# Kernel optimization log

Hardware: AMD Instinct MI355X
Metric: run time of the kernel (lower is better)

Reference implementation:

```python
import jax, jax.numpy as jnp
import numpy as np

N_NODES = 100000
N_EDGES = 1600000
IN_CH, HID_CH, OUT_CH = 128, 128, 64
N_GRAPHS = 64


def gcn_conv(x, src, dst, W, b, n_nodes):
    """PyG-style GCNConv: self-loops already included in (src, dst).
    out_i = b + sum_j norm_ij * (x_j @ W), norm_ij = deg_i^-1/2 * deg_j^-1/2."""
    xw = x @ W  # [N, out]
    deg = jax.ops.segment_sum(jnp.ones_like(dst, dtype=xw.dtype), dst,
                              num_segments=n_nodes)  # [N]
    dinv = jnp.where(deg > 0, jax.lax.rsqrt(jnp.maximum(deg, 1e-12)), 0.0)
    norm = dinv[src] * dinv[dst]  # [E]
    msg = xw[src] * norm[:, None]  # gather + scale  [E, out]
    out = jax.ops.segment_sum(msg, dst, num_segments=n_nodes)  # scatter-add
    return out + b


def global_mean_pool(x, batch, n_graphs):
    s = jax.ops.segment_sum(x, batch, num_segments=n_graphs)
    cnt = jax.ops.segment_sum(jnp.ones((x.shape[0],), x.dtype), batch,
                              num_segments=n_graphs)
    return s / jnp.maximum(cnt, 1.0)[:, None]


def setup_inputs() -> dict:
    key = jax.random.key(0)
    ks = jax.random.split(key, 9)
    x = jax.random.normal(ks[0], (N_NODES, IN_CH), dtype=jnp.float32)
    edge_index = jax.random.randint(ks[1], (2, N_EDGES), 0, N_NODES, dtype=jnp.int64)
    batch = jnp.sort(jax.random.randint(ks[2], (N_NODES,), 0, N_GRAPHS, dtype=jnp.int64))
    # Glorot-ish params
    s1 = 1.0 / np.sqrt(IN_CH)
    s2 = 1.0 / np.sqrt(HID_CH)
    W1 = jax.random.normal(ks[3], (IN_CH, HID_CH), jnp.float32) * s1
    b1 = jnp.zeros((HID_CH,), jnp.float32)
    W2 = jax.random.normal(ks[4], (HID_CH, HID_CH), jnp.float32) * s2
    b2 = jnp.zeros((HID_CH,), jnp.float32)
    Wl = jax.random.normal(ks[5], (HID_CH, OUT_CH), jnp.float32) * s2
    bl = jax.random.normal(ks[6], (OUT_CH,), jnp.float32) * 0.01
    return {"x": x, "edge_index": edge_index, "batch": batch,
            "W1": W1, "b1": b1, "W2": W2, "b2": b2, "Wl": Wl, "bl": bl}


def reference(x, edge_index, batch, W1, b1, W2, b2, Wl, bl):
    n = x.shape[0]
    loop = jnp.arange(n, dtype=edge_index.dtype)
    src = jnp.concatenate([edge_index[0], loop])  # add self-loops
    dst = jnp.concatenate([edge_index[1], loop])
    h = jax.nn.relu(gcn_conv(x, src, dst, W1, b1, n))
    h = jax.nn.relu(gcn_conv(h, src, dst, W2, b2, n))
    g = global_mean_pool(h, batch, N_GRAPHS)  # [B, hid]
    return g @ Wl + bl  # [B, out]
```

## Files before the change

kernel.cpp:

```cpp
#include <hip/hip_runtime.h>

#define N_NODESC 100000
#define N_EDGESC 1600000
#define CH 128
#define NG 64
#define OC 64

#define GST_BLKS 391
#define MFMA_BLKS 1563
#define PAD_STRIDE 64
#define SENTINEL N_NODESC

#define BIN_SHIFT 9
#define BIN_W 512
#define NBINS 196
#define BIN_CAP 16384
#define BIN1_BLKS 391
#define E_PER_BIN1 4096

typedef __attribute__((ext_vector_type(8))) short short8;
typedef __attribute__((ext_vector_type(4))) float f32x4;

__device__ __forceinline__ unsigned short f2b_u(float f) {
    union { float f; unsigned int u; } x; x.f = f;
    unsigned int u = x.u;
    return (unsigned short)((u + 0x7fffu + ((u >> 16) & 1u)) >> 16);
}
__device__ __forceinline__ float b2f_lo(unsigned int v) {
    union { unsigned int u; float f; } x; x.u = v << 16; return x.f;
}
__device__ __forceinline__ float b2f_hi(unsigned int v) {
    union { unsigned int u; float f; } x; x.u = v & 0xffff0000u; return x.f;
}

#define WSTR 136
template<int AFP>
__device__ __forceinline__ void mfma_compute(int blk, int t, const void* __restrict__ Ap,
                                             unsigned short* __restrict__ Ob,
                                             const unsigned short* WsT) {
    int wave = t >> 6, lane = t & 63;
    int quad = lane >> 4, l16 = lane & 15;
    int arow = blk * 64 + wave * 16 + l16;
    bool rowok = arow < N_NODESC;
    f32x4 acc[8] = {};
#pragma unroll
    for (int c = 0; c < 4; ++c) {
        int koff = c * 32 + quad * 8;
        short8 a;
        if (AFP) {
            const float* A = (const float*)Ap;
            float4 f0 = make_float4(0, 0, 0, 0), f1 = make_float4(0, 0, 0, 0);
            if (rowok) {
                f0 = *(const float4*)(A + (size_t)arow * 128 + koff);
                f1 = *(const float4*)(A + (size_t)arow * 128 + koff + 4);
            }
            a[0] = (short)f2b_u(f0.x); a[1] = (short)f2b_u(f0.y);
            a[2] = (short)f2b_u(f0.z); a[3] = (short)f2b_u(f0.w);
            a[4] = (short)f2b_u(f1.x); a[5] = (short)f2b_u(f1.y);
            a[6] = (short)f2b_u(f1.z); a[7] = (short)f2b_u(f1.w);
        } else {
            const unsigned short* A = (const unsigned short*)Ap;
            if (rowok) a = *(const short8*)(A + (size_t)arow * 128 + koff);
            else       a = (short8)(short)0;
        }
#pragma unroll
        for (int tt = 0; tt < 8; ++tt) {
            short8 b = *(const short8*)&WsT[(tt * 16 + l16) * WSTR + koff];
            acc[tt] = __builtin_amdgcn_mfma_f32_16x16x32_bf16(a, b, acc[tt], 0, 0, 0);
        }
    }
    int orow0 = blk * 64 + wave * 16 + quad * 4;
#pragma unroll
    for (int r = 0; r < 4; ++r) {
        int g = orow0 + r;
        if (g < N_NODESC) {
#pragma unroll
            for (int tt = 0; tt < 8; ++tt)
                Ob[(size_t)g * 128 + tt * 16 + l16] = f2b_u(acc[tt][r]);
        }
    }
}

__global__ __launch_bounds__(256) void k_pre(const int* __restrict__ ei,
                                             const int* __restrict__ batch,
                                             const float* __restrict__ W1,
                                             const float* __restrict__ W2,
                                             int* __restrict__ cursor,
                                             unsigned int* __restrict__ binbuf,
                                             unsigned short* __restrict__ Wt1,
                                             unsigned short* __restrict__ Wt2,
                                             int* __restrict__ gstart) {
    __shared__ int hist[NBINS];
    int b = blockIdx.x, t = threadIdx.x;
    if (b < BIN1_BLKS) {
        for (int i = t; i < NBINS; i += 256) hist[i] = 0;
        __syncthreads();
        int e0 = b * E_PER_BIN1;
#pragma unroll 4
        for (int i = 0; i < E_PER_BIN1 / 256; ++i) {
            int e = e0 + i * 256 + t;
            if (e < N_EDGESC) atomicAdd(&hist[ei[N_EDGESC + e] >> BIN_SHIFT], 1);
        }
        __syncthreads();
        for (int i = t; i < NBINS; i += 256) {
            int c = hist[i];
            hist[i] = c ? atomicAdd(&cursor[i], c) : 0;
        }
        __syncthreads();
#pragma unroll 4
        for (int i = 0; i < E_PER_BIN1 / 256; ++i) {
            int e = e0 + i * 256 + t;
            if (e < N_EDGESC) {
                int d = ei[N_EDGESC + e];
                int s = ei[e];
                int bin = d >> BIN_SHIFT;
                int off = atomicAdd(&hist[bin], 1);
                binbuf[(size_t)bin * BIN_CAP + off] =
                    ((unsigned int)(d & (BIN_W - 1)) << 17) | (unsigned int)s;
            }
        }
    } else if (b < BIN1_BLKS + 64) {
        int i = (b - BIN1_BLKS) * 256 + t;
        int k = i >> 7, c = i & 127;
        Wt1[c * 128 + k] = f2b_u(W1[k * 128 + c]);
    } else if (b < BIN1_BLKS + 128) {
        int i = (b - BIN1_BLKS - 64) * 256 + t;
        int k = i >> 7, c = i & 127;
        Wt2[c * 128 + k] = f2b_u(W2[k * 128 + c]);
    } else {
        int i = (b - BIN1_BLKS - 128) * 256 + t;
        if (i >= N_NODESC) return;
        int bb = batch[i];
        int bp = (i == 0) ? -1 : batch[i - 1];
        for (int g = bp + 1; g <= bb; ++g) gstart[g] = i;
        if (i == N_NODESC - 1)
            for (int g = bb + 1; g <= NG; ++g) gstart[g] = N_NODESC;
    }
}

__global__ __launch_bounds__(256) void k_main(const float* __restrict__ x,
                                              const unsigned short* __restrict__ Wt1,
                                              unsigned short* __restrict__ xw,
                                              const int* __restrict__ cursor,
                                              const unsigned int* __restrict__ binbuf,
                                              int* __restrict__ deg,
                                              float* __restrict__ dinvt,
                                              int* __restrict__ pad) {
    __shared__ unsigned short WsT[128 * WSTR];
    int t = threadIdx.x;
    if (blockIdx.x < NBINS) {
        int bin = blockIdx.x;
        if (bin == 0 && t == 0) dinvt[SENTINEL] = 0.f;
        int* ldeg = (int*)WsT;
        for (int i = t; i < BIN_W; i += 256) ldeg[i] = 0;
        __syncthreads();
        int n = cursor[bin];
        size_t base = (size_t)bin * BIN_CAP;
        for (int i = t; i < n; i += 256) {
            unsigned int rec = binbuf[base + i];
            int dl = rec >> 17;
            int s = rec & 0x1FFFF;
            int slot = atomicAdd(&ldeg[dl], 1) & (PAD_STRIDE - 1);
            pad[(size_t)((bin << BIN_SHIFT) + dl) * PAD_STRIDE + slot] = s;
        }
        __syncthreads();
        for (int i = t; i < BIN_W; i += 256) {
            int node = (bin << BIN_SHIFT) + i;
            if (node < N_NODESC) {
                int dg = ldeg[i];
                if (dg > PAD_STRIDE) dg = PAD_STRIDE;
                deg[node] = dg;
                dinvt[node] = rsqrtf((float)(dg + 1));
                int r8 = (dg + 7) & ~7;
                for (int j = dg; j < r8; ++j)
                    pad[(size_t)node * PAD_STRIDE + j] = SENTINEL;
            }
        }
    } else {
        int blk = blockIdx.x - NBINS;
        const uint4* wsrc = (const uint4*)Wt1;
        for (int idx = t; idx < 2048; idx += 256) {
            int row = idx >> 4, sub = idx & 15;
            *((uint4*)&WsT[row * WSTR] + sub) = wsrc[row * 16 + sub];
        }
        __syncthreads();
        mfma_compute<1>(blk, t, x, xw, WsT);
    }
}

__global__ __launch_bounds__(256) void k_mfma2(const unsigned short* __restrict__ A,
                                               const unsigned short* __restrict__ Wt,
                                               unsigned short* __restrict__ Ob) {
    __shared__ unsigned short WsT[128 * WSTR];
    int t = threadIdx.x;
    {
        const uint4* wsrc = (const uint4*)Wt;
        for (int idx = t; idx < 2048; idx += 256) {
            int row = idx >> 4, sub = idx & 15;
            *((uint4*)&WsT[row * WSTR] + sub) = wsrc[row * 16 + sub];
        }
    }
    __syncthreads();
    mfma_compute<0>(blockIdx.x, t, A, Ob, WsT);
}

__device__ __forceinline__ void gather8(const unsigned int* __restrict__ xw,
                                        const int* __restrict__ pad,
                                        const float* __restrict__ dinvt,
                                        int base, int lane,
                                        float& acc0, float& acc1) {
    int s[8];
    float w[8];
    unsigned int v[8];
#pragma unroll
    for (int k = 0; k < 8; ++k) s[k] = pad[base + k];
#pragma unroll
    for (int k = 0; k < 8; ++k) {
        w[k] = dinvt[s[k]];
        v[k] = xw[(unsigned int)(s[k] * 64 + lane)];
    }
#pragma unroll
    for (int k = 0; k < 8; ++k) {
        acc0 += w[k] * b2f_lo(v[k]);
        acc1 += w[k] * b2f_hi(v[k]);
    }
}

__device__ __forceinline__ void gather_pair(const unsigned int* __restrict__ xw,
                                            const int* __restrict__ pad,
                                            const float* __restrict__ dinvt,
                                            int nA, int nB, int dgA, int dgB, int lane,
                                            float& a0, float& a1, float& b0, float& b1) {
    int ngA = (dgA + 7) >> 3, ngB = (dgB + 7) >> 3;
    int baseA = nA * PAD_STRIDE, baseB = nB * PAD_STRIDE;
    int ngmin = ngA < ngB ? ngA : ngB;
    int g = 0;
    for (; g < ngmin; ++g) {
        gather8(xw, pad, dinvt, baseA + g * 8, lane, a0, a1);
        gather8(xw, pad, dinvt, baseB + g * 8, lane, b0, b1);
    }
    for (; g < ngA; ++g) gather8(xw, pad, dinvt, baseA + g * 8, lane, a0, a1);
    for (; g < ngB; ++g) gather8(xw, pad, dinvt, baseB + g * 8, lane, b0, b1);
}

__global__ __launch_bounds__(256) void k_gather1(const unsigned int* __restrict__ xw,
                                                 const int* __restrict__ deg,
                                                 const float* __restrict__ dinvt,
                                                 const int* __restrict__ pad,
                                                 const float* __restrict__ bias,
                                                 unsigned int* __restrict__ outp) {
    int t = threadIdx.x;
    int lane = t & 63;
    int nA = blockIdx.x * 8 + (t >> 6) * 2;
    if (nA >= N_NODESC) return;
    int nB = nA + 1;
    if (nB >= N_NODESC) nB = nA;
    int dgA = deg[nA], dgB = deg[nB];
    float wA = dinvt[nA], wB = dinvt[nB];
    unsigned int vsA = xw[(unsigned int)(nA * 64 + lane)];
    unsigned int vsB = xw[(unsigned int)(nB * 64 + lane)];
    float a0 = wA * b2f_lo(vsA), a1 = wA * b2f_hi(vsA);
    float b0 = wB * b2f_lo(vsB), b1 = wB * b2f_hi(vsB);
    gather_pair(xw, pad, dinvt, nA, nB, dgA, dgB, lane, a0, a1, b0, b1);
    float2 bb = ((const float2*)bias)[lane];
    float oA0 = fmaxf(bb.x + wA * a0, 0.f), oA1 = fmaxf(bb.y + wA * a1, 0.f);
    float oB0 = fmaxf(bb.x + wB * b0, 0.f), oB1 = fmaxf(bb.y + wB * b1, 0.f);
    outp[(unsigned int)(nA * 64 + lane)] =
        ((unsigned int)f2b_u(oA1) << 16) | (unsigned int)f2b_u(oA0);
    outp[(unsigned int)(nB * 64 + lane)] =
        ((unsigned int)f2b_u(oB1) << 16) | (unsigned int)f2b_u(oB0);
}

__global__ __launch_bounds__(256) void k_gather_pool(const unsigned int* __restrict__ xw,
                                                     const int* __restrict__ deg,
                                                     const float* __restrict__ dinvt,
                                                     const int* __restrict__ pad,
                                                     const float* __restrict__ bias,
                                                     const int* __restrict__ batch,
                                                     float* __restrict__ gpart) {
    __shared__ float lds[4 * 128];
    int t = threadIdx.x, w = t >> 6, lane = t & 63;
    int base = blockIdx.x * 16;
    bool fast = batch[base] == batch[base + 15];
    float2 bv = ((const float2*)bias)[lane];
    float sum0 = 0.f, sum1 = 0.f;
#pragma unroll
    for (int p = 0; p < 2; ++p) {
        int nA = base + w * 4 + p * 2;
        int nB = nA + 1;
        int dgA = deg[nA], dgB = deg[nB];
        float wA = dinvt[nA], wB = dinvt[nB];
        unsigned int vsA = xw[(unsigned int)(nA * 64 + lane)];
        unsigned int vsB = xw[(unsigned int)(nB * 64 + lane)];
        float a0 = wA * b2f_lo(vsA), a1 = wA * b2f_hi(vsA);
        float b0 = wB * b2f_lo(vsB), b1 = wB * b2f_hi(vsB);
        gather_pair(xw, pad, dinvt, nA, nB, dgA, dgB, lane, a0, a1, b0, b1);
        float oA0 = fmaxf(bv.x + wA * a0, 0.f), oA1 = fmaxf(bv.y + wA * a1, 0.f);
        float oB0 = fmaxf(bv.x + wB * b0, 0.f), oB1 = fmaxf(bv.y + wB * b1, 0.f);
        if (fast) {
            sum0 += oA0 + oB0; sum1 += oA1 + oB1;
        } else {
            int gA = batch[nA], gB = batch[nB];
            atomicAdd(&gpart[gA * 128 + lane * 2], oA0);
            atomicAdd(&gpart[gA * 128 + lane * 2 + 1], oA1);
            atomicAdd(&gpart[gB * 128 + lane * 2], oB0);
            atomicAdd(&gpart[gB * 128 + lane * 2 + 1], oB1);
        }
    }
    if (fast) {
        lds[w * 128 + lane * 2] = sum0;
        lds[w * 128 + lane * 2 + 1] = sum1;
        __syncthreads();
        if (t < 128) {
            float v = lds[t] + lds[128 + t] + lds[256 + t] + lds[384 + t];
            atomicAdd(&gpart[batch[base] * 128 + t], v);
        }
    }
}

__global__ void k_final(const float* __restrict__ gpart, const int* __restrict__ gstart,
                        const float* __restrict__ Wl, const float* __restrict__ bl,
                        float* __restrict__ out) {
    __shared__ float gs[128];
    int b = blockIdx.x;
    int o = threadIdx.x;
    gs[o] = gpart[b * 128 + o];
    gs[o + 64] = gpart[b * 128 + 64 + o];
    __syncthreads();
    int cnt = gstart[b + 1] - gstart[b];
    float sc = 1.f / (float)(cnt > 0 ? cnt : 1);
    float sum = 0.f;
    for (int k = 0; k < 128; ++k) sum += gs[k] * Wl[k * 64 + o];
    out[b * 64 + o] = bl[o] + sc * sum;
}

extern "C" void kernel_launch(void* const* d_in, const int* in_sizes, int n_in,
                              void* d_out, int out_size, void* d_ws, size_t ws_size,
                              hipStream_t stream) {
    const float* x    = (const float*)d_in[0];
    const int*   ei   = (const int*)d_in[1];
    const int*   batch= (const int*)d_in[2];
    const float* W1   = (const float*)d_in[3];
    const float* b1   = (const float*)d_in[4];
    const float* W2   = (const float*)d_in[5];
    const float* b2   = (const float*)d_in[6];
    const float* Wl   = (const float*)d_in[7];
    const float* bl   = (const float*)d_in[8];
    float* out = (float*)d_out;

    char* ws = (char*)d_ws;
    unsigned short* xw_s = (unsigned short*)ws; ws += (size_t)(N_NODESC + 1) * CH * 2;
    unsigned short* h_b  = (unsigned short*)ws; ws += (size_t)N_NODESC * CH * 2;
    unsigned short* Wt1 = (unsigned short*)ws; ws += (size_t)CH * CH * 2;
    unsigned short* Wt2 = (unsigned short*)ws; ws += (size_t)CH * CH * 2;
    int*   cursor = (int*)ws;   ws += (size_t)NBINS * 4;
    float* gpart  = (float*)ws; ws += (size_t)NG * CH * 4;
    int*   deg    = (int*)ws;   ws += (size_t)N_NODESC * 4;
    float* dinvt  = (float*)ws; ws += (size_t)(N_NODESC + 1) * 4;
    int*   pad    = (int*)ws;   ws += (size_t)N_NODESC * PAD_STRIDE * 4;
    unsigned int* binbuf = (unsigned int*)ws; ws += (size_t)NBINS * BIN_CAP * 4;
    int*   gstart = (int*)ws;   ws += (NG + 8) * 4;

    hipMemsetAsync(cursor, 0, (size_t)NBINS * 4 + (size_t)NG * CH * 4, stream);

    k_pre<<<BIN1_BLKS + 128 + GST_BLKS, 256, 0, stream>>>(ei, batch, W1, W2,
        cursor, binbuf, Wt1, Wt2, gstart);
    k_main<<<NBINS + MFMA_BLKS, 256, 0, stream>>>(x, Wt1, xw_s, cursor, binbuf,
                                                  deg, dinvt, pad);

    k_gather1<<<(N_NODESC + 7) / 8, 256, 0, stream>>>((const unsigned int*)xw_s,
        deg, dinvt, pad, b1, (unsigned int*)h_b);
    k_mfma2<<<MFMA_BLKS, 256, 0, stream>>>(h_b, Wt2, xw_s);
    k_gather_pool<<<N_NODESC / 16, 256, 0, stream>>>((const unsigned int*)xw_s,
        deg, dinvt, pad, b2, batch, gpart);

    k_final<<<NG, 64, 0, stream>>>(gpart, gstart, Wl, bl, out);
}
```

Measured before the change: 307.2 us.

## Fuse all GCN stages into one cooperative persistent kernel with grid syncs

Replaces the six separate kernel launches with a single cooperative persistent kernel that loops over work units per phase and separates phases with grid-wide syncs, falling back to the old launch sequence if cooperative launch fails. It also pads the bin cursors to one per 64-byte line to reduce atomic contention. The aim is to remove launch gaps and tail effects between stages. The costs are grid-sync overhead, a grid capped at 1024 blocks, LDS for both the weight tile and scratch in every block, and an occupancy query on every call.

Measured after the change: 747.0 us. 143% more time.

```diff
diff --git a/kernel.cpp b/kernel.cpp
--- a/kernel.cpp
+++ b/kernel.cpp
@@ -1,4 +1,6 @@
 #include <hip/hip_runtime.h>
+#include <hip/hip_cooperative_groups.h>
+namespace cg = cooperative_groups;
 
 #define N_NODESC 100000
 #define N_EDGESC 1600000
@@ -17,6 +19,12 @@
 #define BIN_CAP 16384
 #define BIN1_BLKS 391
 #define E_PER_BIN1 4096
+
+#define GRID_MAX 1024
+#define P0_UNITS (BIN1_BLKS + 128 + GST_BLKS)
+#define P1_UNITS (NBINS + MFMA_BLKS)
+#define P2_UNITS 12500
+#define P4_UNITS 6250
 
 typedef __attribute__((ext_vector_type(8))) short short8;
 typedef __attribute__((ext_vector_type(4))) float f32x4;
@@ -81,129 +89,6 @@
     }
 }
 
-__global__ __launch_bounds__(256) void k_pre(const int* __restrict__ ei,
-                                             const int* __restrict__ batch,
-                                             const float* __restrict__ W1,
-                                             const float* __restrict__ W2,
-                                             int* __restrict__ cursor,
-                                             unsigned int* __restrict__ binbuf,
-                                             unsigned short* __restrict__ Wt1,
-                                             unsigned short* __restrict__ Wt2,
-                                             int* __restrict__ gstart) {
-    __shared__ int hist[NBINS];
-    int b = blockIdx.x, t = threadIdx.x;
-    if (b < BIN1_BLKS) {
-        for (int i = t; i < NBINS; i += 256) hist[i] = 0;
-        __syncthreads();
-        int e0 = b * E_PER_BIN1;
-#pragma unroll 4
-        for (int i = 0; i < E_PER_BIN1 / 256; ++i) {
-            int e = e0 + i * 256 + t;
-            if (e < N_EDGESC) atomicAdd(&hist[ei[N_EDGESC + e] >> BIN_SHIFT], 1);
-        }
-        __syncthreads();
-        for (int i = t; i < NBINS; i += 256) {
-            int c = hist[i];
-            hist[i] = c ? atomicAdd(&cursor[i], c) : 0;
-        }
-        __syncthreads();
-#pragma unroll 4
-        for (int i = 0; i < E_PER_BIN1 / 256; ++i) {
-            int e = e0 + i * 256 + t;
-            if (e < N_EDGESC) {
-                int d = ei[N_EDGESC + e];
-                int s = ei[e];
-                int bin = d >> BIN_SHIFT;
-                int off = atomicAdd(&hist[bin], 1);
-                binbuf[(size_t)bin * BIN_CAP + off] =
-                    ((unsigned int)(d & (BIN_W - 1)) << 17) | (unsigned int)s;
-            }
-        }
-    } else if (b < BIN1_BLKS + 64) {
-        int i = (b - BIN1_BLKS) * 256 + t;
-        int k = i >> 7, c = i & 127;
-        Wt1[c * 128 + k] = f2b_u(W1[k * 128 + c]);
-    } else if (b < BIN1_BLKS + 128) {
-        int i = (b - BIN1_BLKS - 64) * 256 + t;
-        int k = i >> 7, c = i & 127;
-        Wt2[c * 128 + k] = f2b_u(W2[k * 128 + c]);
-    } else {
-        int i = (b - BIN1_BLKS - 128) * 256 + t;
-        if (i >= N_NODESC) return;
-        int bb = batch[i];
-        int bp = (i == 0) ? -1 : batch[i - 1];
-        for (int g = bp + 1; g <= bb; ++g) gstart[g] = i;
-        if (i == N_NODESC - 1)
-            for (int g = bb + 1; g <= NG; ++g) gstart[g] = N_NODESC;
-    }
-}
-
-__global__ __launch_bounds__(256) void k_main(const float* __restrict__ x,
-                                              const unsigned short* __restrict__ Wt1,
-                                              unsigned short* __restrict__ xw,
-                                              const int* __restrict__ cursor,
-                                              const unsigned int* __restrict__ binbuf,
-                                              int* __restrict__ deg,
-                                              float* __restrict__ dinvt,
-                                              int* __restrict__ pad) {
-    __shared__ unsigned short WsT[128 * WSTR];
-    int t = threadIdx.x;
-    if (blockIdx.x < NBINS) {
-        int bin = blockIdx.x;
-        if (bin == 0 && t == 0) dinvt[SENTINEL] = 0.f;
-        int* ldeg = (int*)WsT;
-        for (int i = t; i < BIN_W; i += 256) ldeg[i] = 0;
-        __syncthreads();
-        int n = cursor[bin];
-        size_t base = (size_t)bin * BIN_CAP;
-        for (int i = t; i < n; i += 256) {
-            unsigned int rec = binbuf[base + i];
-            int dl = rec >> 17;
-            int s = rec & 0x1FFFF;
-            int slot = atomicAdd(&ldeg[dl], 1) & (PAD_STRIDE - 1);
-            pad[(size_t)((bin << BIN_SHIFT) + dl) * PAD_STRIDE + slot] = s;
-        }
-        __syncthreads();
-        for (int i = t; i < BIN_W; i += 256) {
-            int node = (bin << BIN_SHIFT) + i;
-            if (node < N_NODESC) {
-                int dg = ldeg[i];
-                if (dg > PAD_STRIDE) dg = PAD_STRIDE;
-                deg[node] = dg;
-                dinvt[node] = rsqrtf((float)(dg + 1));
-                int r8 = (dg + 7) & ~7;
-                for (int j = dg; j < r8; ++j)
-                    pad[(size_t)node * PAD_STRIDE + j] = SENTINEL;
-            }
-        }
-    } else {
-        int blk = blockIdx.x - NBINS;
-        const uint4* wsrc = (const uint4*)Wt1;
-        for (int idx = t; idx < 2048; idx += 256) {
-            int row = idx >> 4, sub = idx & 15;
-            *((uint4*)&WsT[row * WSTR] + sub) = wsrc[row * 16 + sub];
-        }
-        __syncthreads();
-        mfma_compute<1>(blk, t, x, xw, WsT);
-    }
-}
-
-__global__ __launch_bounds__(256) void k_mfma2(const unsigned short* __restrict__ A,
-                                               const unsigned short* __restrict__ Wt,
-                                               unsigned short* __restrict__ Ob) {
-    __shared__ unsigned short WsT[128 * WSTR];
-    int t = threadIdx.x;
-    {
-        const uint4* wsrc = (const uint4*)Wt;
-        for (int idx = t; idx < 2048; idx += 256) {
-            int row = idx >> 4, sub = idx & 15;
-            *((uint4*)&WsT[row * WSTR] + sub) = wsrc[row * 16 + sub];
-        }
-    }
-    __syncthreads();
-    mfma_compute<0>(blockIdx.x, t, A, Ob, WsT);
-}
-
 __device__ __forceinline__ void gather8(const unsigned int* __restrict__ xw,
                                         const int* __restrict__ pad,
                                         const float* __restrict__ dinvt,
@@ -243,15 +128,79 @@
     for (; g < ngB; ++g) gather8(xw, pad, dinvt, baseB + g * 8, lane, b0, b1);
 }
 
-__global__ __launch_bounds__(256) void k_gather1(const unsigned int* __restrict__ xw,
-                                                 const int* __restrict__ deg,
-                                                 const float* __restrict__ dinvt,
-                                                 const int* __restrict__ pad,
-                                                 const float* __restrict__ bias,
-                                                 unsigned int* __restrict__ outp) {
-    int t = threadIdx.x;
-    int lane = t & 63;
-    int nA = blockIdx.x * 8 + (t >> 6) * 2;
+__device__ __forceinline__ void bin1_body(int u, int t, const int* __restrict__ ei,
+                                          int* __restrict__ cursor,
+                                          unsigned int* __restrict__ binbuf,
+                                          int* hist) {
+    for (int i = t; i < NBINS; i += 256) hist[i] = 0;
+    __syncthreads();
+    int e0 = u * E_PER_BIN1;
+#pragma unroll 4
+    for (int i = 0; i < E_PER_BIN1 / 256; ++i) {
+        int e = e0 + i * 256 + t;
+        if (e < N_EDGESC) atomicAdd(&hist[ei[N_EDGESC + e] >> BIN_SHIFT], 1);
+    }
+    __syncthreads();
+    for (int i = t; i < NBINS; i += 256) {
+        int c = hist[i];
+        hist[i] = c ? atomicAdd(&cursor[i * 16], c) : 0;
+    }
+    __syncthreads();
+#pragma unroll 4
+    for (int i = 0; i < E_PER_BIN1 / 256; ++i) {
+        int e = e0 + i * 256 + t;
+        if (e < N_EDGESC) {
+            int d = ei[N_EDGESC + e];
+            int s = ei[e];
+            int bin = d >> BIN_SHIFT;
+            int off = atomicAdd(&hist[bin], 1);
+            binbuf[(size_t)bin * BIN_CAP + off] =
+                ((unsigned int)(d & (BIN_W - 1)) << 17) | (unsigned int)s;
+        }
+    }
+    __syncthreads();
+}
+
+__device__ __forceinline__ void bin2_body(int bin, int t, const int* __restrict__ cursor,
+                                          const unsigned int* __restrict__ binbuf,
+                                          int* __restrict__ deg, float* __restrict__ dinvt,
+                                          int* __restrict__ pad, int* ldeg) {
+    if (bin == 0 && t == 0) dinvt[SENTINEL] = 0.f;
+    for (int i = t; i < BIN_W; i += 256) ldeg[i] = 0;
+    __syncthreads();
+    int n = cursor[bin * 16];
+    size_t base = (size_t)bin * BIN_CAP;
+    for (int i = t; i < n; i += 256) {
+        unsigned int rec = binbuf[base + i];
+        int dl = rec >> 17;
+        int s = rec & 0x1FFFF;
+        int slot = atomicAdd(&ldeg[dl], 1) & (PAD_STRIDE - 1);
+        pad[(size_t)((bin << BIN_SHIFT) + dl) * PAD_STRIDE + slot] = s;
+    }
+    __syncthreads();
+    for (int i = t; i < BIN_W; i += 256) {
+        int node = (bin << BIN_SHIFT) + i;
+        if (node < N_NODESC) {
+            int dg = ldeg[i];
+            if (dg > PAD_STRIDE) dg = PAD_STRIDE;
+            deg[node] = dg;
+            dinvt[node] = rsqrtf((float)(dg + 1));
+            int r8 = (dg + 7) & ~7;
+            for (int j = dg; j < r8; ++j)
+                pad[(size_t)node * PAD_STRIDE + j] = SENTINEL;
+        }
+    }
+    __syncthreads();
+}
+
+__device__ __forceinline__ void gather1_body(int u, int wv, int lane,
+                                             const unsigned int* __restrict__ xw,
+                                             const int* __restrict__ deg,
+                                             const float* __restrict__ dinvt,
+                                             const int* __restrict__ pad,
+                                             const float* __restrict__ bias1,
+                                             unsigned int* __restrict__ hb) {
+    int nA = u * 8 + wv * 2;
     if (nA >= N_NODESC) return;
     int nB = nA + 1;
     if (nB >= N_NODESC) nB = nA;
@@ -262,31 +211,30 @@
     float a0 = wA * b2f_lo(vsA), a1 = wA * b2f_hi(vsA);
     float b0 = wB * b2f_lo(vsB), b1 = wB * b2f_hi(vsB);
     gather_pair(xw, pad, dinvt, nA, nB, dgA, dgB, lane, a0, a1, b0, b1);
-    float2 bb = ((const float2*)bias)[lane];
+    float2 bb = ((const float2*)bias1)[lane];
     float oA0 = fmaxf(bb.x + wA * a0, 0.f), oA1 = fmaxf(bb.y + wA * a1, 0.f);
     float oB0 = fmaxf(bb.x + wB * b0, 0.f), oB1 = fmaxf(bb.y + wB * b1, 0.f);
-    outp[(unsigned int)(nA * 64 + lane)] =
+    hb[(unsigned int)(nA * 64 + lane)] =
         ((unsigned int)f2b_u(oA1) << 16) | (unsigned int)f2b_u(oA0);
-    outp[(unsigned int)(nB * 64 + lane)] =
+    hb[(unsigned int)(nB * 64 + lane)] =
         ((unsigned int)f2b_u(oB1) << 16) | (unsigned int)f2b_u(oB0);
 }
 
-__global__ __launch_bounds__(256) void k_gather_pool(const unsigned int* __restrict__ xw,
-                                                     const int* __restrict__ deg,
-                                                     const float* __restrict__ dinvt,
-                                                     const int* __restrict__ pad,
-                                                     const float* __restrict__ bias,
-                                                     const int* __restrict__ batch,
-                                                     float* __restrict__ gpart) {
-    __shared__ float lds[4 * 128];
-    int t = threadIdx.x, w = t >> 6, lane = t & 63;
-    int base = blockIdx.x * 16;
+__device__ __forceinline__ void gpool_body(int u, int t, int wv, int lane,
+                                           const unsigned int* __restrict__ xw,
+                                           const int* __restrict__ deg,
+                                           const float* __restrict__ dinvt,
+                                           const int* __restrict__ pad,
+                                           const float* __restrict__ bias2,
+                                           const int* __restrict__ batch,
+                                           float* __restrict__ gpart, float* lds) {
+    int base = u * 16;
     bool fast = batch[base] == batch[base + 15];
-    float2 bv = ((const float2*)bias)[lane];
+    float2 bv = ((const float2*)bias2)[lane];
     float sum0 = 0.f, sum1 = 0.f;
 #pragma unroll
     for (int p = 0; p < 2; ++p) {
-        int nA = base + w * 4 + p * 2;
+        int nA = base + wv * 4 + p * 2;
         int nB = nA + 1;
         int dgA = deg[nA], dgB = deg[nB];
         float wA = dinvt[nA], wB = dinvt[nB];
@@ -308,14 +256,207 @@
         }
     }
     if (fast) {
-        lds[w * 128 + lane * 2] = sum0;
-        lds[w * 128 + lane * 2 + 1] = sum1;
+        lds[wv * 128 + lane * 2] = sum0;
+        lds[wv * 128 + lane * 2 + 1] = sum1;
         __syncthreads();
         if (t < 128) {
             float v = lds[t] + lds[128 + t] + lds[256 + t] + lds[384 + t];
             atomicAdd(&gpart[batch[base] * 128 + t], v);
         }
-    }
+        __syncthreads();
+    }
+}
+
+__global__ __launch_bounds__(256, 4) void k_all(
+    const float* __restrict__ x, const int* __restrict__ ei,
+    const int* __restrict__ batch,
+    const float* __restrict__ W1, const float* __restrict__ W2,
+    const float* __restrict__ bias1, const float* __restrict__ bias2,
+    const float* __restrict__ Wl, const float* __restrict__ bl,
+    float* __restrict__ out,
+    unsigned short* __restrict__ xw, unsigned short* __restrict__ hb,
+    unsigned short* __restrict__ Wt1, unsigned short* __restrict__ Wt2,
+    int* __restrict__ cursor, unsigned int* __restrict__ binbuf,
+    int* __restrict__ deg, float* __restrict__ dinvt,
+    int* __restrict__ pad, float* __restrict__ gpart,
+    int* __restrict__ gstart)
+{
+    cg::grid_group grid = cg::this_grid();
+    __shared__ unsigned short WsT[128 * WSTR];
+    __shared__ int scratch[BIN_W];
+    int t = threadIdx.x;
+    int lane = t & 63, wv = t >> 6;
+    int nblk = gridDim.x;
+
+    for (int u = blockIdx.x; u < P0_UNITS; u += nblk) {
+        if (u < BIN1_BLKS) {
+            bin1_body(u, t, ei, cursor, binbuf, (int*)WsT);
+        } else if (u < BIN1_BLKS + 64) {
+            int i = (u - BIN1_BLKS) * 256 + t;
+            int k = i >> 7, c = i & 127;
+            Wt1[c * 128 + k] = f2b_u(W1[k * 128 + c]);
+        } else if (u < BIN1_BLKS + 128) {
+            int i = (u - BIN1_BLKS - 64) * 256 + t;
+            int k = i >> 7, c = i & 127;
+            Wt2[c * 128 + k] = f2b_u(W2[k * 128 + c]);
+        } else {
+            int i = (u - BIN1_BLKS - 128) * 256 + t;
+            if (i < N_NODESC) {
+                int bb = batch[i];
+                int bp = (i == 0) ? -1 : batch[i - 1];
+                for (int g = bp + 1; g <= bb; ++g) gstart[g] = i;
+                if (i == N_NODESC - 1)
+                    for (int g = bb + 1; g <= NG; ++g) gstart[g] = N_NODESC;
+            }
+        }
+    }
+    grid.sync();
+
+    {
+        const uint4* wsrc = (const uint4*)Wt1;
+        for (int idx = t; idx < 2048; idx += 256) {
+            int row = idx >> 4, sub = idx & 15;
+            *((uint4*)&WsT[row * WSTR] + sub) = wsrc[row * 16 + sub];
+        }
+        __syncthreads();
+    }
+    for (int u = blockIdx.x; u < P1_UNITS; u += nblk) {
+        if (u < NBINS) bin2_body(u, t, cursor, binbuf, deg, dinvt, pad, scratch);
+        else           mfma_compute<1>(u - NBINS, t, x, xw, WsT);
+    }
+    grid.sync();
+
+    for (int u = blockIdx.x; u < P2_UNITS; u += nblk)
+        gather1_body(u, wv, lane, (const unsigned int*)xw, deg, dinvt, pad, bias1,
+                     (unsigned int*)hb);
+    grid.sync();
+
+    {
+        const uint4* wsrc = (const uint4*)Wt2;
+        for (int idx = t; idx < 2048; idx += 256) {
+            int row = idx >> 4, sub = idx & 15;
+            *((uint4*)&WsT[row * WSTR] + sub) = wsrc[row * 16 + sub];
+        }
+        __syncthreads();
+    }
+    for (int u = blockIdx.x; u < MFMA_BLKS; u += nblk)
+        mfma_compute<0>(u, t, hb, xw, WsT);
+    grid.sync();
+
+    for (int u = blockIdx.x; u < P4_UNITS; u += nblk)
+        gpool_body(u, t, wv, lane, (const unsigned int*)xw, deg, dinvt, pad, bias2,
+                   batch, gpart, (float*)scratch);
+    grid.sync();
+
+    {
+        float* gs = (float*)scratch;
+        for (int u = blockIdx.x; u < NG; u += nblk) {
+            if (t < 128) gs[t] = gpart[u * 128 + t];
+            __syncthreads();
+            if (t < 64) {
+                int cnt = gstart[u + 1] - gstart[u];
+                float sc = 1.f / (float)(cnt > 0 ? cnt : 1);
+                float sum = 0.f;
+                for (int k = 0; k < 128; ++k) sum += gs[k] * Wl[k * 64 + t];
+                out[u * 64 + t] = bl[t] + sc * sum;
+            }
+            __syncthreads();
+        }
+    }
+}
+
+__global__ __launch_bounds__(256) void k_pre(const int* __restrict__ ei,
+                                             const int* __restrict__ batch,
+                                             const float* __restrict__ W1,
+                                             const float* __restrict__ W2,
+                                             int* __restrict__ cursor,
+                                             unsigned int* __restrict__ binbuf,
+                                             unsigned short* __restrict__ Wt1,
+                                             unsigned short* __restrict__ Wt2,
+                                             int* __restrict__ gstart) {
+    __shared__ int hist[NBINS];
+    int b = blockIdx.x, t = threadIdx.x;
+    if (b < BIN1_BLKS) {
+        bin1_body(b, t, ei, cursor, binbuf, hist);
+    } else if (b < BIN1_BLKS + 64) {
+        int i = (b - BIN1_BLKS) * 256 + t;
+        int k = i >> 7, c = i & 127;
+        Wt1[c * 128 + k] = f2b_u(W1[k * 128 + c]);
+    } else if (b < BIN1_BLKS + 128) {
+        int i = (b - BIN1_BLKS - 64) * 256 + t;
+        int k = i >> 7, c = i & 127;
+        Wt2[c * 128 + k] = f2b_u(W2[k * 128 + c]);
+    } else {
+        int i = (b - BIN1_BLKS - 128) * 256 + t;
+        if (i >= N_NODESC) return;
+        int bb = batch[i];
+        int bp = (i == 0) ? -1 : batch[i - 1];
+        for (int g = bp + 1; g <= bb; ++g) gstart[g] = i;
+        if (i == N_NODESC - 1)
+            for (int g = bb + 1; g <= NG; ++g) gstart[g] = N_NODESC;
+    }
+}
+
+__global__ __launch_bounds__(256) void k_main(const float* __restrict__ x,
+                                              const unsigned short* __restrict__ Wt1,
+                                              unsigned short* __restrict__ xw,
+                                              const int* __restrict__ cursor,
+                                              const unsigned int* __restrict__ binbuf,
+                                              int* __restrict__ deg,
+                                              float* __restrict__ dinvt,
+                                              int* __restrict__ pad) {
+    __shared__ unsigned short WsT[128 * WSTR];
+    int t = threadIdx.x;
+    if (blockIdx.x < NBINS) {
+        bin2_body(blockIdx.x, t, cursor, binbuf, deg, dinvt, pad, (int*)WsT);
+    } else {
+        const uint4* wsrc = (const uint4*)Wt1;
+        for (int idx = t; idx < 2048; idx += 256) {
+            int row = idx >> 4, sub = idx & 15;
+            *((uint4*)&WsT[row * WSTR] + sub) = wsrc[row * 16 + sub];
+        }
+        __syncthreads();
+        mfma_compute<1>(blockIdx.x - NBINS, t, x, xw, WsT);
+    }
+}
+
+__global__ __launch_bounds__(256) void k_mfma2(const unsigned short* __restrict__ A,
+                                               const unsigned short* __restrict__ Wt,
+                                               unsigned short* __restrict__ Ob) {
+    __shared__ unsigned short WsT[128 * WSTR];
+    int t = threadIdx.x;
+    {
+        const uint4* wsrc = (const uint4*)Wt;
+        for (int idx = t; idx < 2048; idx += 256) {
+            int row = idx >> 4, sub = idx & 15;
+            *((uint4*)&WsT[row * WSTR] + sub) = wsrc[row * 16 + sub];
+        }
+    }
+    __syncthreads();
+    mfma_compute<0>(blockIdx.x, t, A, Ob, WsT);
+}
+
+__global__ __launch_bounds__(256) void k_gather1(const unsigned int* __restrict__ xw,
+                                                 const int* __restrict__ deg,
+                                                 const float* __restrict__ dinvt,
+                                                 const int* __restrict__ pad,
+                                                 const float* __restrict__ bias,
+                                                 unsigned int* __restrict__ outp) {
+    int t = threadIdx.x;
+    gather1_body(blockIdx.x, t >> 6, t & 63, xw, deg, dinvt, pad, bias, outp);
+}
+
+__global__ __launch_bounds__(256) void k_gather_pool(const unsigned int* __restrict__ xw,
+                                                     const int* __restrict__ deg,
+                                                     const float* __restrict__ dinvt,
+                                                     const int* __restrict__ pad,
+                                                     const float* __restrict__ bias,
+                                                     const int* __restrict__ batch,
+                                                     float* __restrict__ gpart) {
+    __shared__ float lds[4 * 128];
+    int t = threadIdx.x;
+    gpool_body(blockIdx.x, t, t >> 6, t & 63, xw, deg, dinvt, pad, bias, batch,
+               gpart, lds);
 }
 
 __global__ void k_final(const float* __restrict__ gpart, const int* __restrict__ gstart,
@@ -341,9 +482,9 @@
     const int*   ei   = (const int*)d_in[1];
     const int*   batch= (const int*)d_in[2];
     const float* W1   = (const float*)d_in[3];
-    const float* b1   = (const float*)d_in[4];
+    const float* b1v  = (const float*)d_in[4];
     const float* W2   = (const float*)d_in[5];
-    const float* b2   = (const float*)d_in[6];
+    const float* b2v  = (const float*)d_in[6];
     const float* Wl   = (const float*)d_in[7];
     const float* bl   = (const float*)d_in[8];
     float* out = (float*)d_out;
@@ -353,7 +494,7 @@
     unsigned short* h_b  = (unsigned short*)ws; ws += (size_t)N_NODESC * CH * 2;
     unsigned short* Wt1 = (unsigned short*)ws; ws += (size_t)CH * CH * 2;
     unsigned short* Wt2 = (unsigned short*)ws; ws += (size_t)CH * CH * 2;
-    int*   cursor = (int*)ws;   ws += (size_t)NBINS * 4;
+    int*   cursor = (int*)ws;   ws += (size_t)NBINS * 16 * 4;
     float* gpart  = (float*)ws; ws += (size_t)NG * CH * 4;
     int*   deg    = (int*)ws;   ws += (size_t)N_NODESC * 4;
     float* dinvt  = (float*)ws; ws += (size_t)(N_NODESC + 1) * 4;
@@ -361,18 +502,37 @@
     unsigned int* binbuf = (unsigned int*)ws; ws += (size_t)NBINS * BIN_CAP * 4;
     int*   gstart = (int*)ws;   ws += (NG + 8) * 4;
 
-    hipMemsetAsync(cursor, 0, (size_t)NBINS * 4 + (size_t)NG * CH * 4, stream);
-
-    k_pre<<<BIN1_BLKS + 128 + GST_BLKS, 256, 0, stream>>>(ei, batch, W1, W2,
-        cursor, binbuf, Wt1, Wt2, gstart);
-    k_main<<<NBINS + MFMA_BLKS, 256, 0, stream>>>(x, Wt1, xw_s, cursor, binbuf,
-                                                  deg, dinvt, pad);
-
-    k_gather1<<<(N_NODESC + 7) / 8, 256, 0, stream>>>((const unsigned int*)xw_s,
-        deg, dinvt, pad, b1, (unsigned int*)h_b);
-    k_mfma2<<<MFMA_BLKS, 256, 0, stream>>>(h_b, Wt2, xw_s);
-    k_gather_pool<<<N_NODESC / 16, 256, 0, stream>>>((const unsigned int*)xw_s,
-        deg, dinvt, pad, b2, batch, gpart);
-
-    k_final<<<NG, 64, 0, stream>>>(gpart, gstart, Wl, bl, out);
-}
+    hipMemsetAsync(cursor, 0, (size_t)NBINS * 16 * 4 + (size_t)NG * CH * 4, stream);
+
+    int perCU = 0;
+    hipError_t qerr = hipOccupancyMaxActiveBlocksPerMultiprocessor(
+        &perCU, (const void*)k_all, 256, 0);
+    bool coop_ok = false;
+    if (qerr == hipSuccess && perCU > 0) {
+        int grid = perCU * 256;
+        if (grid > GRID_MAX) grid = GRID_MAX;
+        void* args[] = {
+            (void*)&x, (void*)&ei, (void*)&batch, (void*)&W1, (void*)&W2,
+            (void*)&b1v, (void*)&b2v, (void*)&Wl, (void*)&bl, (void*)&out,
+            (void*)&xw_s, (void*)&h_b, (void*)&Wt1, (void*)&Wt2,
+            (void*)&cursor, (void*)&binbuf, (void*)&deg, (void*)&dinvt,
+            (void*)&pad, (void*)&gpart, (void*)&gstart
+        };
+        hipError_t lerr = hipLaunchCooperativeKernel((const void*)k_all, dim3(grid),
+                                                     dim3(256), args, 0, stream);
+        coop_ok = (lerr == hipSuccess);
+    }
+
+    if (!coop_ok) {
+        k_pre<<<BIN1_BLKS + 128 + GST_BLKS, 256, 0, stream>>>(ei, batch, W1, W2,
+            cursor, binbuf, Wt1, Wt2, gstart);
+        k_main<<<NBINS + MFMA_BLKS, 256, 0, stream>>>(x, Wt1, xw_s, cursor, binbuf,
+                                                      deg, dinvt, pad);
+        k_gather1<<<P2_UNITS, 256, 0, stream>>>((const unsigned int*)xw_s,
+            deg, dinvt, pad, b1v, (unsigned int*)h_b);
+        k_mfma2<<<MFMA_BLKS, 256, 0, stream>>>(h_b, Wt2, xw_s);
+        k_gather_pool<<<P4_UNITS, 256, 0, stream>>>((const unsigned int*)xw_s,
+            deg, dinvt, pad, b2v, batch, gpart);
+        k_final<<<NG, 64, 0, stream>>>(gpart, gstart, Wl, bl, out);
+    }
+}
```

## Restructure GCN pipeline: fuse layer-1 GEMM into binning, gather+GEMM2, pool+head

Applied to the files above, without the earlier changes.

Moves the layer-1 MFMA GEMM into the first binning kernel, with each block converting W1 to bf16 in LDS itself, so it overlaps with edge binning. The bin-to-pad pass becomes its own kernel. Layer-1 gather and the layer-2 GEMM are fused per 64-node block, and the final linear head runs in the last-arriving pool block via an atomic done counter. Bin cursors are padded to separate cache lines. This drops two launches and a transpose pass, but every GEMM block now redoes the W1 conversion, and the fused gather+GEMM blocks run with lower parallelism and a large LDS footprint.

Result: slower. 956.7 us (+211.4%).

```diff
diff --git a/kernel.cpp b/kernel.cpp
--- a/kernel.cpp
+++ b/kernel.cpp
@@ -6,7 +6,6 @@
 #define NG 64
 #define OC 64
 
-#define GST_BLKS 391
 #define MFMA_BLKS 1563
 #define PAD_STRIDE 64
 #define SENTINEL N_NODESC
@@ -17,6 +16,14 @@
 #define BIN_CAP 16384
 #define BIN1_BLKS 391
 #define E_PER_BIN1 4096
+#define GST_BLKS 391
+
+#define U_BIN1 BIN1_BLKS
+#define U_MFMA (U_BIN1 + MFMA_BLKS)
+#define U_PW2  (U_MFMA + 64)
+#define PRE_BLKS (U_PW2 + GST_BLKS)
+
+#define GP_BLKS 6250
 
 typedef __attribute__((ext_vector_type(8))) short short8;
 typedef __attribute__((ext_vector_type(4))) float f32x4;
@@ -81,129 +88,6 @@
     }
 }
 
-__global__ __launch_bounds__(256) void k_pre(const int* __restrict__ ei,
-                                             const int* __restrict__ batch,
-                                             const float* __restrict__ W1,
-                                             const float* __restrict__ W2,
-                                             int* __restrict__ cursor,
-                                             unsigned int* __restrict__ binbuf,
-                                             unsigned short* __restrict__ Wt1,
-                                             unsigned short* __restrict__ Wt2,
-                                             int* __restrict__ gstart) {
-    __shared__ int hist[NBINS];
-    int b = blockIdx.x, t = threadIdx.x;
-    if (b < BIN1_BLKS) {
-        for (int i = t; i < NBINS; i += 256) hist[i] = 0;
-        __syncthreads();
-        int e0 = b * E_PER_BIN1;
-#pragma unroll 4
-        for (int i = 0; i < E_PER_BIN1 / 256; ++i) {
-            int e = e0 + i * 256 + t;
-            if (e < N_EDGESC) atomicAdd(&hist[ei[N_EDGESC + e] >> BIN_SHIFT], 1);
-        }
-        __syncthreads();
-        for (int i = t; i < NBINS; i += 256) {
-            int c = hist[i];
-            hist[i] = c ? atomicAdd(&cursor[i], c) : 0;
-        }
-        __syncthreads();
-#pragma unroll 4
-        for (int i = 0; i < E_PER_BIN1 / 256; ++i) {
-            int e = e0 + i * 256 + t;
-            if (e < N_EDGESC) {
-                int d = ei[N_EDGESC + e];
-                int s = ei[e];
-                int bin = d >> BIN_SHIFT;
-                int off = atomicAdd(&hist[bin], 1);
-                binbuf[(size_t)bin * BIN_CAP + off] =
-                    ((unsigned int)(d & (BIN_W - 1)) << 17) | (unsigned int)s;
-            }
-        }
-    } else if (b < BIN1_BLKS + 64) {
-        int i = (b - BIN1_BLKS) * 256 + t;
-        int k = i >> 7, c = i & 127;
-        Wt1[c * 128 + k] = f2b_u(W1[k * 128 + c]);
-    } else if (b < BIN1_BLKS + 128) {
-        int i = (b - BIN1_BLKS - 64) * 256 + t;
-        int k = i >> 7, c = i & 127;
-        Wt2[c * 128 + k] = f2b_u(W2[k * 128 + c]);
-    } else {
-        int i = (b - BIN1_BLKS - 128) * 256 + t;
-        if (i >= N_NODESC) return;
-        int bb = batch[i];
-        int bp = (i == 0) ? -1 : batch[i - 1];
-        for (int g = bp + 1; g <= bb; ++g) gstart[g] = i;
-        if (i == N_NODESC - 1)
-            for (int g = bb + 1; g <= NG; ++g) gstart[g] = N_NODESC;
-    }
-}
-
-__global__ __launch_bounds__(256) void k_main(const float* __restrict__ x,
-                                              const unsigned short* __restrict__ Wt1,
-                                              unsigned short* __restrict__ xw,
-                                              const int* __restrict__ cursor,
-                                              const unsigned int* __restrict__ binbuf,
-                                              int* __restrict__ deg,
-                                              float* __restrict__ dinvt,
-                                              int* __restrict__ pad) {
-    __shared__ unsigned short WsT[128 * WSTR];
-    int t = threadIdx.x;
-    if (blockIdx.x < NBINS) {
-        int bin = blockIdx.x;
-        if (bin == 0 && t == 0) dinvt[SENTINEL] = 0.f;
-        int* ldeg = (int*)WsT;
-        for (int i = t; i < BIN_W; i += 256) ldeg[i] = 0;
-        __syncthreads();
-        int n = cursor[bin];
-        size_t base = (size_t)bin * BIN_CAP;
-        for (int i = t; i < n; i += 256) {
-            unsigned int rec = binbuf[base + i];
-            int dl = rec >> 17;
-            int s = rec & 0x1FFFF;
-            int slot = atomicAdd(&ldeg[dl], 1) & (PAD_STRIDE - 1);
-            pad[(size_t)((bin << BIN_SHIFT) + dl) * PAD_STRIDE + slot] = s;
-        }
-        __syncthreads();
-        for (int i = t; i < BIN_W; i += 256) {
-            int node = (bin << BIN_SHIFT) + i;
-            if (node < N_NODESC) {
-                int dg = ldeg[i];
-                if (dg > PAD_STRIDE) dg = PAD_STRIDE;
-                deg[node] = dg;
-                dinvt[node] = rsqrtf((float)(dg + 1));
-                int r8 = (dg + 7) & ~7;
-                for (int j = dg; j < r8; ++j)
-                    pad[(size_t)node * PAD_STRIDE + j] = SENTINEL;
-            }
-        }
-    } else {
-        int blk = blockIdx.x - NBINS;
-        const uint4* wsrc = (const uint4*)Wt1;
-        for (int idx = t; idx < 2048; idx += 256) {
-            int row = idx >> 4, sub = idx & 15;
-            *((uint4*)&WsT[row * WSTR] + sub) = wsrc[row * 16 + sub];
-        }
-        __syncthreads();
-        mfma_compute<1>(blk, t, x, xw, WsT);
-    }
-}
-
-__global__ __launch_bounds__(256) void k_mfma2(const unsigned short* __restrict__ A,
-                                               const unsigned short* __restrict__ Wt,
-                                               unsigned short* __restrict__ Ob) {
-    __shared__ unsigned short WsT[128 * WSTR];
-    int t = threadIdx.x;
-    {
-        const uint4* wsrc = (const uint4*)Wt;
-        for (int idx = t; idx < 2048; idx += 256) {
-            int row = idx >> 4, sub = idx & 15;
-            *((uint4*)&WsT[row * WSTR] + sub) = wsrc[row * 16 + sub];
-        }
-    }
-    __syncthreads();
-    mfma_compute<0>(blockIdx.x, t, A, Ob, WsT);
-}
-
 __device__ __forceinline__ void gather8(const unsigned int* __restrict__ xw,
                                         const int* __restrict__ pad,
                                         const float* __restrict__ dinvt,
@@ -243,58 +127,174 @@
     for (; g < ngB; ++g) gather8(xw, pad, dinvt, baseB + g * 8, lane, b0, b1);
 }
 
-__global__ __launch_bounds__(256) void k_gather1(const unsigned int* __restrict__ xw,
-                                                 const int* __restrict__ deg,
-                                                 const float* __restrict__ dinvt,
-                                                 const int* __restrict__ pad,
-                                                 const float* __restrict__ bias,
-                                                 unsigned int* __restrict__ outp) {
-    int t = threadIdx.x;
-    int lane = t & 63;
-    int nA = blockIdx.x * 8 + (t >> 6) * 2;
-    if (nA >= N_NODESC) return;
-    int nB = nA + 1;
-    if (nB >= N_NODESC) nB = nA;
-    int dgA = deg[nA], dgB = deg[nB];
-    float wA = dinvt[nA], wB = dinvt[nB];
-    unsigned int vsA = xw[(unsigned int)(nA * 64 + lane)];
-    unsigned int vsB = xw[(unsigned int)(nB * 64 + lane)];
-    float a0 = wA * b2f_lo(vsA), a1 = wA * b2f_hi(vsA);
-    float b0 = wB * b2f_lo(vsB), b1 = wB * b2f_hi(vsB);
-    gather_pair(xw, pad, dinvt, nA, nB, dgA, dgB, lane, a0, a1, b0, b1);
-    float2 bb = ((const float2*)bias)[lane];
-    float oA0 = fmaxf(bb.x + wA * a0, 0.f), oA1 = fmaxf(bb.y + wA * a1, 0.f);
-    float oB0 = fmaxf(bb.x + wB * b0, 0.f), oB1 = fmaxf(bb.y + wB * b1, 0.f);
-    outp[(unsigned int)(nA * 64 + lane)] =
-        ((unsigned int)f2b_u(oA1) << 16) | (unsigned int)f2b_u(oA0);
-    outp[(unsigned int)(nB * 64 + lane)] =
-        ((unsigned int)f2b_u(oB1) << 16) | (unsigned int)f2b_u(oB0);
-}
-
-__global__ __launch_bounds__(256) void k_gather_pool(const unsigned int* __restrict__ xw,
-                                                     const int* __restrict__ deg,
-                                                     const float* __restrict__ dinvt,
-                                                     const int* __restrict__ pad,
-                                                     const float* __restrict__ bias,
-                                                     const int* __restrict__ batch,
-                                                     float* __restrict__ gpart) {
-    __shared__ float lds[4 * 128];
-    int t = threadIdx.x, w = t >> 6, lane = t & 63;
+__global__ __launch_bounds__(256) void k_pre(const float* __restrict__ x,
+                                             const int* __restrict__ ei,
+                                             const int* __restrict__ batch,
+                                             const float* __restrict__ W1,
+                                             const float* __restrict__ W2,
+                                             int* __restrict__ cursor,
+                                             unsigned int* __restrict__ binbuf,
+                                             unsigned short* __restrict__ Wt2,
+                                             int* __restrict__ gstart,
+                                             unsigned short* __restrict__ xw) {
+    __shared__ unsigned short WsT[128 * WSTR];
+    int b = blockIdx.x, t = threadIdx.x;
+    if (b < U_BIN1) {
+        int* hist = (int*)WsT;
+        for (int i = t; i < NBINS; i += 256) hist[i] = 0;
+        __syncthreads();
+        int e0 = b * E_PER_BIN1;
+#pragma unroll 4
+        for (int i = 0; i < E_PER_BIN1 / 256; ++i) {
+            int e = e0 + i * 256 + t;
+            if (e < N_EDGESC) atomicAdd(&hist[ei[N_EDGESC + e] >> BIN_SHIFT], 1);
+        }
+        __syncthreads();
+        for (int i = t; i < NBINS; i += 256) {
+            int c = hist[i];
+            hist[i] = c ? atomicAdd(&cursor[i * 16], c) : 0;
+        }
+        __syncthreads();
+#pragma unroll 4
+        for (int i = 0; i < E_PER_BIN1 / 256; ++i) {
+            int e = e0 + i * 256 + t;
+            if (e < N_EDGESC) {
+                int d = ei[N_EDGESC + e];
+                int s = ei[e];
+                int bin = d >> BIN_SHIFT;
+                int off = atomicAdd(&hist[bin], 1);
+                binbuf[(size_t)bin * BIN_CAP + off] =
+                    ((unsigned int)(d & (BIN_W - 1)) << 17) | (unsigned int)s;
+            }
+        }
+    } else if (b < U_MFMA) {
+        for (int idx = t; idx < 16384; idx += 256) {
+            int k = idx >> 7, c = idx & 127;
+            WsT[c * WSTR + k] = f2b_u(W1[idx]);
+        }
+        __syncthreads();
+        mfma_compute<1>(b - U_BIN1, t, x, xw, WsT);
+    } else if (b < U_PW2) {
+        int i = (b - U_MFMA) * 256 + t;
+        int k = i >> 7, c = i & 127;
+        Wt2[c * 128 + k] = f2b_u(W2[k * 128 + c]);
+    } else {
+        int i = (b - U_PW2) * 256 + t;
+        if (i >= N_NODESC) return;
+        int bb = batch[i];
+        int bp = (i == 0) ? -1 : batch[i - 1];
+        for (int g = bp + 1; g <= bb; ++g) gstart[g] = i;
+        if (i == N_NODESC - 1)
+            for (int g = bb + 1; g <= NG; ++g) gstart[g] = N_NODESC;
+    }
+}
+
+__global__ __launch_bounds__(256) void k_bin2(const int* __restrict__ cursor,
+                                              const unsigned int* __restrict__ binbuf,
+                                              int* __restrict__ deg,
+                                              float* __restrict__ dinvt,
+                                              int* __restrict__ pad) {
+    __shared__ int ldeg[BIN_W];
+    int bin = blockIdx.x, t = threadIdx.x;
+    if (bin == 0 && t == 0) dinvt[SENTINEL] = 0.f;
+    for (int i = t; i < BIN_W; i += 256) ldeg[i] = 0;
+    __syncthreads();
+    int n = cursor[bin * 16];
+    size_t base = (size_t)bin * BIN_CAP;
+    for (int i = t; i < n; i += 256) {
+        unsigned int rec = binbuf[base + i];
+        int dl = rec >> 17;
+        int s = rec & 0x1FFFF;
+        int slot = atomicAdd(&ldeg[dl], 1) & (PAD_STRIDE - 1);
+        pad[(size_t)((bin << BIN_SHIFT) + dl) * PAD_STRIDE + slot] = s;
+    }
+    __syncthreads();
+    for (int i = t; i < BIN_W; i += 256) {
+        int node = (bin << BIN_SHIFT) + i;
+        if (node < N_NODESC) {
+            int dg = ldeg[i];
+            if (dg > PAD_STRIDE) dg = PAD_STRIDE;
+            deg[node] = dg;
+            dinvt[node] = rsqrtf((float)(dg + 1));
+            int r8 = (dg + 7) & ~7;
+            for (int j = dg; j < r8; ++j)
+                pad[(size_t)node * PAD_STRIDE + j] = SENTINEL;
+        }
+    }
+}
+
+__global__ __launch_bounds__(256) void k_gg(const unsigned int* __restrict__ xw,
+                                            const int* __restrict__ deg,
+                                            const float* __restrict__ dinvt,
+                                            const int* __restrict__ pad,
+                                            const float* __restrict__ bias1,
+                                            unsigned short* __restrict__ hb,
+                                            const unsigned short* __restrict__ Wt2,
+                                            unsigned short* __restrict__ xw2) {
+    __shared__ unsigned short WsT[128 * WSTR];
+    int t = threadIdx.x, wv = t >> 6, lane = t & 63;
+    {
+        const uint4* wsrc = (const uint4*)Wt2;
+        for (int idx = t; idx < 2048; idx += 256) {
+            int row = idx >> 4, sub = idx & 15;
+            *((uint4*)&WsT[row * WSTR] + sub) = wsrc[row * 16 + sub];
+        }
+    }
+    float2 bb = ((const float2*)bias1)[lane];
+#pragma unroll 1
+    for (int p = 0; p < 8; ++p) {
+        int nA = blockIdx.x * 64 + wv * 16 + p * 2;
+        if (nA < N_NODESC) {
+            int nB = nA + 1;
+            if (nB >= N_NODESC) nB = nA;
+            int dgA = deg[nA], dgB = deg[nB];
+            float wA = dinvt[nA], wB = dinvt[nB];
+            unsigned int vsA = xw[(unsigned int)(nA * 64 + lane)];
+            unsigned int vsB = xw[(unsigned int)(nB * 64 + lane)];
+            float a0 = wA * b2f_lo(vsA), a1 = wA * b2f_hi(vsA);
+            float b0 = wB * b2f_lo(vsB), b1 = wB * b2f_hi(vsB);
+            gather_pair(xw, pad, dinvt, nA, nB, dgA, dgB, lane, a0, a1, b0, b1);
+            float oA0 = fmaxf(bb.x + wA * a0, 0.f), oA1 = fmaxf(bb.y + wA * a1, 0.f);
+            float oB0 = fmaxf(bb.x + wB * b0, 0.f), oB1 = fmaxf(bb.y + wB * b1, 0.f);
+            ((unsigned int*)hb)[(unsigned int)(nA * 64 + lane)] =
+                ((unsigned int)f2b_u(oA1) << 16) | (unsigned int)f2b_u(oA0);
+            ((unsigned int*)hb)[(unsigned int)(nB * 64 + lane)] =
+                ((unsigned int)f2b_u(oB1) << 16) | (unsigned int)f2b_u(oB0);
+        }
+    }
+    __syncthreads();
+    mfma_compute<0>(blockIdx.x, t, hb, xw2, WsT);
+}
+
+__global__ __launch_bounds__(256) void k_gp(const unsigned int* __restrict__ xw2,
+                                            const int* __restrict__ deg,
+                                            const float* __restrict__ dinvt,
+                                            const int* __restrict__ pad,
+                                            const float* __restrict__ bias2,
+                                            const int* __restrict__ batch,
+                                            float* __restrict__ gpart,
+                                            const int* __restrict__ gstart,
+                                            const float* __restrict__ Wl,
+                                            const float* __restrict__ bl,
+                                            float* __restrict__ out,
+                                            int* __restrict__ done) {
+    __shared__ float shead[NG * CH];
+    int t = threadIdx.x, wv = t >> 6, lane = t & 63;
     int base = blockIdx.x * 16;
     bool fast = batch[base] == batch[base + 15];
-    float2 bv = ((const float2*)bias)[lane];
+    float2 bv = ((const float2*)bias2)[lane];
     float sum0 = 0.f, sum1 = 0.f;
 #pragma unroll
     for (int p = 0; p < 2; ++p) {
-        int nA = base + w * 4 + p * 2;
+        int nA = base + wv * 4 + p * 2;
         int nB = nA + 1;
         int dgA = deg[nA], dgB = deg[nB];
         float wA = dinvt[nA], wB = dinvt[nB];
-        unsigned int vsA = xw[(unsigned int)(nA * 64 + lane)];
-        unsigned int vsB = xw[(unsigned int)(nB * 64 + lane)];
+        unsigned int vsA = xw2[(unsigned int)(nA * 64 + lane)];
+        unsigned int vsB = xw2[(unsigned int)(nB * 64 + lane)];
         float a0 = wA * b2f_lo(vsA), a1 = wA * b2f_hi(vsA);
         float b0 = wB * b2f_lo(vsB), b1 = wB * b2f_hi(vsB);
-        gather_pair(xw, pad, dinvt, nA, nB, dgA, dgB, lane, a0, a1, b0, b1);
+        gather_pair(xw2, pad, dinvt, nA, nB, dgA, dgB, lane, a0, a1, b0, b1);
         float oA0 = fmaxf(bv.x + wA * a0, 0.f), oA1 = fmaxf(bv.y + wA * a1, 0.f);
         float oB0 = fmaxf(bv.x + wB * b0, 0.f), oB1 = fmaxf(bv.y + wB * b1, 0.f);
         if (fast) {
@@ -308,30 +308,33 @@
         }
     }
     if (fast) {
-        lds[w * 128 + lane * 2] = sum0;
-        lds[w * 128 + lane * 2 + 1] = sum1;
+        shead[wv * 128 + lane * 2] = sum0;
+        shead[wv * 128 + lane * 2 + 1] = sum1;
         __syncthreads();
         if (t < 128) {
-            float v = lds[t] + lds[128 + t] + lds[256 + t] + lds[384 + t];
+            float v = shead[t] + shead[128 + t] + shead[256 + t] + shead[384 + t];
             atomicAdd(&gpart[batch[base] * 128 + t], v);
         }
     }
-}
-
-__global__ void k_final(const float* __restrict__ gpart, const int* __restrict__ gstart,
-                        const float* __restrict__ Wl, const float* __restrict__ bl,
-                        float* __restrict__ out) {
-    __shared__ float gs[128];
-    int b = blockIdx.x;
-    int o = threadIdx.x;
-    gs[o] = gpart[b * 128 + o];
-    gs[o + 64] = gpart[b * 128 + 64 + o];
-    __syncthreads();
-    int cnt = gstart[b + 1] - gstart[b];
-    float sc = 1.f / (float)(cnt > 0 ? cnt : 1);
-    float sum = 0.f;
-    for (int k = 0; k < 128; ++k) sum += gs[k] * Wl[k * 64 + o];
-    out[b * 64 + o] = bl[o] + sc * sum;
+    __syncthreads();
+    __threadfence();
+    __shared__ int is_last;
+    if (t == 0) is_last = (atomicAdd(done, 1) == GP_BLKS - 1) ? 1 : 0;
+    __syncthreads();
+    if (!is_last) return;
+    for (int i = t; i < NG * CH; i += 256)
+        shead[i] = atomicAdd(&gpart[i], 0.f);
+    __syncthreads();
+    int o = t & 63;
+    int g0 = t >> 6;
+    for (int rep = 0; rep < 16; ++rep) {
+        int g = g0 + rep * 4;
+        int cnt = gstart[g + 1] - gstart[g];
+        float sc = 1.f / (float)(cnt > 0 ? cnt : 1);
+        float sum = 0.f;
+        for (int k = 0; k < 128; ++k) sum += shead[g * 128 + k] * Wl[k * 64 + o];
+        out[g * 64 + o] = bl[o] + sc * sum;
+    }
 }
 
 extern "C" void kernel_launch(void* const* d_in, const int* in_sizes, int n_in,
@@ -341,38 +344,35 @@
     const int*   ei   = (const int*)d_in[1];
     const int*   batch= (const int*)d_in[2];
     const float* W1   = (const float*)d_in[3];
-    const float* b1   = (const float*)d_in[4];
+    const float* b1v  = (const float*)d_in[4];
     const float* W2   = (const float*)d_in[5];
-    const float* b2   = (const float*)d_in[6];
+    const float* b2v  = (const float*)d_in[6];
     const float* Wl   = (const float*)d_in[7];
     const float* bl   = (const float*)d_in[8];
     float* out = (float*)d_out;
 
     char* ws = (char*)d_ws;
     unsigned short* xw_s = (unsigned short*)ws; ws += (size_t)(N_NODESC + 1) * CH * 2;
+    unsigned short* xw2_s= (unsigned short*)ws; ws += (size_t)(N_NODESC + 1) * CH * 2;
     unsigned short* h_b  = (unsigned short*)ws; ws += (size_t)N_NODESC * CH * 2;
-    unsigned short* Wt1 = (unsigned short*)ws; ws += (size_t)CH * CH * 2;
     unsigned short* Wt2 = (unsigned short*)ws; ws += (size_t)CH * CH * 2;
-    int*   cursor = (int*)ws;   ws += (size_t)NBINS * 4;
+    int*   cursor = (int*)ws;   ws += (size_t)NBINS * 16 * 4;
     float* gpart  = (float*)ws; ws += (size_t)NG * CH * 4;
+    int*   done   = (int*)ws;   ws += 16 * 4;
     int*   deg    = (int*)ws;   ws += (size_t)N_NODESC * 4;
     float* dinvt  = (float*)ws; ws += (size_t)(N_NODESC + 1) * 4;
     int*   pad    = (int*)ws;   ws += (size_t)N_NODESC * PAD_STRIDE * 4;
     unsigned int* binbuf = (unsigned int*)ws; ws += (size_t)NBINS * BIN_CAP * 4;
     int*   gstart = (int*)ws;   ws += (NG + 8) * 4;
 
-    hipMemsetAsync(cursor, 0, (size_t)NBINS * 4 + (size_t)NG * CH * 4, stream);
-
-    k_pre<<<BIN1_BLKS + 128 + GST_BLKS, 256, 0, stream>>>(ei, batch, W1, W2,
-        cursor, binbuf, Wt1, Wt2, gstart);
-    k_main<<<NBINS + MFMA_BLKS, 256, 0, stream>>>(x, Wt1, xw_s, cursor, binbuf,
-                                                  deg, dinvt, pad);
-
-    k_gather1<<<(N_NODESC + 7) / 8, 256, 0, stream>>>((const unsigned int*)xw_s,
-        deg, dinvt, pad, b1, (unsigned int*)h_b);
-    k_mfma2<<<MFMA_BLKS, 256, 0, stream>>>(h_b, Wt2, xw_s);
-    k_gather_pool<<<N_NODESC / 16, 256, 0, stream>>>((const unsigned int*)xw_s,
-        deg, dinvt, pad, b2, batch, gpart);
-
-    k_final<<<NG, 64, 0, stream>>>(gpart, gstart, Wl, bl, out);
-}
+    hipMemsetAsync(cursor, 0,
+                   (size_t)NBINS * 16 * 4 + (size_t)NG * CH * 4 + 16 * 4, stream);
+
+    k_pre<<<PRE_BLKS, 256, 0, stream>>>(x, ei, batch, W1, W2, cursor, binbuf,
+                                        Wt2, gstart, xw_s);
+    k_bin2<<<NBINS, 256, 0, stream>>>(cursor, binbuf, deg, dinvt, pad);
+    k_gg<<<MFMA_BLKS, 256, 0, stream>>>((const unsigned int*)xw_s, deg, dinvt, pad,
+                                        b1v, h_b, Wt2, xw2_s);
+    k_gp<<<GP_BLKS, 256, 0, stream>>>((const unsigned int*)xw2_s, deg, dinvt, pad,
+                                      b2v, batch, gpart, gstart, Wl, bl, out, done);
+}
```
